# Kernel optimization log

Hardware: AMD Instinct MI355X
Metric: run time of the kernel (lower is better)

Reference implementation:

```python
import jax, jax.numpy as jnp
import numpy as np

CHANNELS = 64
WEIGHT_NUMS = [66 * 64, 64 * 64, 64]  # layer0 (C+2)->C, layer1 C->C, layer2 C->1
BIAS_NUMS = [64, 64, 1]
NUM_GEN_PARAMS = sum(WEIGHT_NUMS) + sum(BIAS_NUMS)  # 8513


def setup_inputs() -> dict:
    key = jax.random.key(0)
    k1, k2 = jax.random.split(key)
    N, C, H, W = 4, 64, 80, 200
    num_ins = 8  # instances per image -> M = 32 total
    M = N * num_ins
    x = jax.random.normal(k1, (N, C, H, W), dtype=jnp.float32)
    mask_head_params = jax.random.normal(k2, (M, NUM_GEN_PARAMS), dtype=jnp.float32) * 0.1
    return {"x": x, "mask_head_params": mask_head_params, "num_ins": num_ins}


def reference(x, mask_head_params, num_ins):
    N, C, H, W = x.shape
    ch = CHANNELS
    # compute_locations with stride=1 (stride//2 == 0); source bug divides the
    # whole tensor by W (locations[:1,:,:] /= W on a batch-1 tensor).
    xx, yy = jnp.meshgrid(jnp.arange(W, dtype=x.dtype), jnp.arange(H, dtype=x.dtype), indexing='xy')
    loc = jnp.stack([xx, yy], axis=0) / W  # [2, H, W]
    xa = jnp.concatenate([jnp.broadcast_to(loc[None], (N, 2, H, W)), x], axis=1)  # [N, C+2, H, W]
    feats = jnp.repeat(xa, num_ins, axis=0)  # [M, C+2, H, W] per-instance inputs
    M = feats.shape[0]
    # parse_dynamic_params: split generated params into per-layer weights/biases
    splits = np.cumsum(WEIGHT_NUMS + BIAS_NUMS)[:-1]
    w0, w1, w2, b0, b1, b2 = jnp.split(mask_head_params, splits, axis=1)
    w0 = w0.reshape(M, ch, ch + 2)
    w1 = w1.reshape(M, ch, ch)
    w2 = w2.reshape(M, 1, ch)
    b2 = b2 - 2.19  # mask bias shift (is_mask=True)
    # grouped 1x1 convs (groups=M) as per-instance GEMMs with ReLU between layers
    h = jax.nn.relu(jnp.einsum('mkc,mchw->mkhw', w0, feats) + b0[:, :, None, None])
    h = jax.nn.relu(jnp.einsum('mkc,mchw->mkhw', w1, h) + b1[:, :, None, None])
    out = jnp.einsum('mkc,mchw->mkhw', w2, h) + b2[:, :, None, None]
    return out.reshape(1, -1, H, W)  # [1, M*out_channels, H, W]
```

## Files before the change

kernel.cpp:

```cpp
#include <hip/hip_runtime.h>

typedef __attribute__((ext_vector_type(8))) short    short8;
typedef __attribute__((ext_vector_type(4))) float    f32x4;
typedef __attribute__((ext_vector_type(4))) unsigned uint4_;
typedef __attribute__((ext_vector_type(2))) unsigned uint2_;

#define HW     16000
#define WWID   200
#define NPARAM 8513

__device__ __forceinline__ unsigned f2bf(float f) {
    unsigned u = __builtin_bit_cast(unsigned, f);
    return (u + 0x7FFFu + ((u >> 16) & 1u)) >> 16;
}
__device__ __forceinline__ unsigned pkbf2(float a, float b) {
    return f2bf(a) | (f2bf(b) << 16);
}
__device__ __forceinline__ short8 mk8(unsigned a, unsigned b, unsigned c, unsigned d) {
    uint4_ u; u.x = a; u.y = b; u.z = c; u.w = d;
    return __builtin_bit_cast(short8, u);
}

__global__ __launch_bounds__(512, 1) void condlane_fused(
    const float* __restrict__ x,
    const float* __restrict__ params,
    float* __restrict__ out,
    int num_ins)
{
    extern __shared__ char lds[];
    char* xt = lds;
    const int tid  = threadIdx.x;
    const int lane = tid & 63;
    const int wid  = tid >> 6;
    const int n    = blockIdx.y;
    const int pxg0 = blockIdx.x * 256;
    char* h0a = lds + 65536 + wid * 4096;
    char* h0b = h0a + 2048;

    {
        const int p   = tid & 255;
        const int sel = tid >> 8;
        const int pc  = min(pxg0 + p, HW - 1);
        const float* xp = x + (size_t)n * 64 * HW + pc;
        #pragma unroll
        for (int it = 0; it < 4; ++it) {
            int c0 = sel * 32 + it * 8;
            uint4_ d;
            d.x = pkbf2(xp[(size_t)(c0 + 0) * HW], xp[(size_t)(c0 + 1) * HW]);
            d.y = pkbf2(xp[(size_t)(c0 + 2) * HW], xp[(size_t)(c0 + 3) * HW]);
            d.z = pkbf2(xp[(size_t)(c0 + 4) * HW], xp[(size_t)(c0 + 5) * HW]);
            d.w = pkbf2(xp[(size_t)(c0 + 6) * HW], xp[(size_t)(c0 + 7) * HW]);
            int byte = (p * 256 + c0 * 2) ^ ((p & 15) << 4);
            *(uint4_*)(xt + byte) = d;
        }
        const int pg = pxg0 + p;
        float lx = (float)(pg % WWID) * (1.0f / WWID);
        float ly = (float)(pg / WWID) * (1.0f / WWID);
        uint4_ z; z.x = 0; z.y = 0; z.z = 0; z.w = 0;
        uint4_ cv; cv.x = pkbf2(lx, ly); cv.y = pkbf2(1.0f, 0.0f); cv.z = 0; cv.w = 0;
        int ba = (p * 256 + 128 + sel * 32) ^ ((p & 15) << 4);
        int bb = (p * 256 + 144 + sel * 32) ^ ((p & 15) << 4);
        *(uint4_*)(xt + ba) = (sel == 0) ? cv : z;
        *(uint4_*)(xt + bb) = z;
    }

    const int m  = n * num_ins + wid;
    const int g  = (lane >> 4) & 3;
    const int hi = lane >> 4;
    const float* pm = params + (size_t)m * NPARAM;

    short8 w0f[3][4], w1f[2][4];
    #pragma unroll
    for (int kb = 0; kb < 4; ++kb) {
        const int k = kb * 16 + (lane & 15);
        #pragma unroll
        for (int ch = 0; ch < 2; ++ch) {
            const float* s = pm + k * 66 + 2 + ch * 32 + hi * 8;
            w0f[ch][kb] = mk8(pkbf2(s[0], s[1]), pkbf2(s[2], s[3]),
                              pkbf2(s[4], s[5]), pkbf2(s[6], s[7]));
        }
        {
            float a = (hi == 0) ? pm[k * 66 + 0] : 0.0f;
            float b = (hi == 0) ? pm[k * 66 + 1] : 0.0f;
            float c = (hi == 0) ? pm[8384 + k]   : 0.0f;
            w0f[2][kb] = mk8(pkbf2(a, b), pkbf2(c, 0.0f), 0u, 0u);
        }
        #pragma unroll
        for (int ch = 0; ch < 2; ++ch) {
            const float* s = pm + 4224 + k * 64 + ch * 32 + hi * 8;
            w1f[ch][kb] = mk8(pkbf2(s[0], s[1]), pkbf2(s[2], s[3]),
                              pkbf2(s[4], s[5]), pkbf2(s[6], s[7]));
        }
    }
    f32x4 bias1[4], w2v[4];
    #pragma unroll
    for (int kb = 0; kb < 4; ++kb)
        #pragma unroll
        for (int j = 0; j < 4; ++j) {
            bias1[kb][j] = pm[8448 + kb * 16 + g * 4 + j];
            w2v[kb][j]   = pm[8320 + kb * 16 + g * 4 + j];
        }
    const float b2 = pm[8512] - 2.19f;

    __syncthreads();

    const int nsl = min(16, (HW - pxg0) >> 4);
    const int hpx = lane & 15;
    const int swz = (lane & 15) << 4;

    for (int sA = 0; sA < 8; ++sA) {
        const int sB = sA + 8;
        const int pxlA = sA * 16 + hpx;
        const int pxlB = pxlA + 128;
        short8 xfA[3], xfB[3];
        #pragma unroll
        for (int ch = 0; ch < 3; ++ch) {
            xfA[ch] = *(const short8*)(xt + ((pxlA * 256 + ch * 64 + hi * 16) ^ swz));
            xfB[ch] = *(const short8*)(xt + ((pxlB * 256 + ch * 64 + hi * 16) ^ swz));
        }
        f32x4 acc0A[4], acc0B[4];
        #pragma unroll
        for (int kb = 0; kb < 4; ++kb)
            #pragma unroll
            for (int j = 0; j < 4; ++j) { acc0A[kb][j] = 0.f; acc0B[kb][j] = 0.f; }
        #pragma unroll
        for (int ch = 0; ch < 3; ++ch)
            #pragma unroll
            for (int kb = 0; kb < 4; ++kb) {
                acc0A[kb] = __builtin_amdgcn_mfma_f32_16x16x32_bf16(w0f[ch][kb], xfA[ch], acc0A[kb], 0, 0, 0);
                acc0B[kb] = __builtin_amdgcn_mfma_f32_16x16x32_bf16(w0f[ch][kb], xfB[ch], acc0B[kb], 0, 0, 0);
            }
        #pragma unroll
        for (int kb = 0; kb < 4; ++kb) {
            uint2_ pkA, pkB;
            pkA.x = pkbf2(fmaxf(acc0A[kb][0], 0.f), fmaxf(acc0A[kb][1], 0.f));
            pkA.y = pkbf2(fmaxf(acc0A[kb][2], 0.f), fmaxf(acc0A[kb][3], 0.f));
            pkB.x = pkbf2(fmaxf(acc0B[kb][0], 0.f), fmaxf(acc0B[kb][1], 0.f));
            pkB.y = pkbf2(fmaxf(acc0B[kb][2], 0.f), fmaxf(acc0B[kb][3], 0.f));
            int byte = (hpx * 128 + kb * 32 + g * 8) ^ ((hpx & 7) << 4);
            *(uint2_*)(h0a + byte) = pkA;
            *(uint2_*)(h0b + byte) = pkB;
        }
        short8 hfA[2], hfB[2];
        #pragma unroll
        for (int ch = 0; ch < 2; ++ch) {
            int byte = (hpx * 128 + ch * 64 + hi * 16) ^ ((hpx & 7) << 4);
            hfA[ch] = *(const short8*)(h0a + byte);
            hfB[ch] = *(const short8*)(h0b + byte);
        }
        f32x4 acc1A[4], acc1B[4];
        #pragma unroll
        for (int kb = 0; kb < 4; ++kb) { acc1A[kb] = bias1[kb]; acc1B[kb] = bias1[kb]; }
        #pragma unroll
        for (int ch = 0; ch < 2; ++ch)
            #pragma unroll
            for (int kb = 0; kb < 4; ++kb) {
                acc1A[kb] = __builtin_amdgcn_mfma_f32_16x16x32_bf16(w1f[ch][kb], hfA[ch], acc1A[kb], 0, 0, 0);
                acc1B[kb] = __builtin_amdgcn_mfma_f32_16x16x32_bf16(w1f[ch][kb], hfB[ch], acc1B[kb], 0, 0, 0);
            }
        float vA = 0.f, vB = 0.f;
        #pragma unroll
        for (int kb = 0; kb < 4; ++kb)
            #pragma unroll
            for (int j = 0; j < 4; ++j) {
                vA += w2v[kb][j] * fmaxf(acc1A[kb][j], 0.f);
                vB += w2v[kb][j] * fmaxf(acc1B[kb][j], 0.f);
            }
        vA += __shfl_xor(vA, 16); vA += __shfl_xor(vA, 32);
        vB += __shfl_xor(vB, 16); vB += __shfl_xor(vB, 32);
        if (lane < 16)
            out[(size_t)m * HW + pxg0 + sA * 16 + lane] = vA + b2;
        else if (lane < 32 && sB < nsl)
            out[(size_t)m * HW + pxg0 + sB * 16 + (lane - 16)] = vB + b2;
    }
}

extern "C" void kernel_launch(void* const* d_in, const int* in_sizes, int n_in,
                              void* d_out, int out_size, void* d_ws, size_t ws_size,
                              hipStream_t stream) {
    const float* x      = (const float*)d_in[0];
    const float* params = (const float*)d_in[1];
    float* out          = (float*)d_out;

    const int N = in_sizes[0] / (64 * HW);
    const int M = in_sizes[1] / NPARAM;
    const int num_ins = M / N;

    dim3 grid((HW + 255) / 256, N);
    condlane_fused<<<grid, 512, 98304, stream>>>(x, params, out, num_ins);
}
```

Before: 26.30 us.

## Split output channels across wave pairs with 1024-thread blocks

Doubles the block to 16 waves, so each instance is handled by two waves that each own half of the 64 hidden channels. Layer-0 activations are exchanged through a double-buffered shared h0 tile, and partial layer-2 sums are combined through LDS with a one-step-delayed store. The aim is more waves in flight and fewer registers per wave, for better latency hiding. The cost is a block-wide __syncthreads every pixel slice, and only one 16-pixel slice is processed per iteration instead of two.

```diff
diff --git a/kernel.cpp b/kernel.cpp
--- a/kernel.cpp
+++ b/kernel.cpp
@@ -21,21 +21,26 @@
     return __builtin_bit_cast(short8, u);
 }
 
-__global__ __launch_bounds__(512, 1) void condlane_fused(
+__global__ __launch_bounds__(1024, 4) void condlane_ksplit(
     const float* __restrict__ x,
     const float* __restrict__ params,
     float* __restrict__ out,
-    int num_ins)
+    int num_ins, int M_total)
 {
     extern __shared__ char lds[];
-    char* xt = lds;
+    char*  xt     = lds;
+    char*  h0base = lds + 65536;
+    float* vpart  = (float*)(lds + 65536 + 32768);
+
     const int tid  = threadIdx.x;
     const int lane = tid & 63;
     const int wid  = tid >> 6;
+    const int inst = wid >> 1;
+    const int kh   = wid & 1;
     const int n    = blockIdx.y;
     const int pxg0 = blockIdx.x * 256;
-    char* h0a = lds + 65536 + wid * 4096;
-    char* h0b = h0a + 2048;
+    const int g    = (lane >> 4) & 3;
+    const int px16 = lane & 15;
 
     {
         const int p   = tid & 255;
@@ -43,8 +48,8 @@
         const int pc  = min(pxg0 + p, HW - 1);
         const float* xp = x + (size_t)n * 64 * HW + pc;
         #pragma unroll
-        for (int it = 0; it < 4; ++it) {
-            int c0 = sel * 32 + it * 8;
+        for (int it = 0; it < 2; ++it) {
+            int c0 = sel * 16 + it * 8;
             uint4_ d;
             d.x = pkbf2(xp[(size_t)(c0 + 0) * HW], xp[(size_t)(c0 + 1) * HW]);
             d.y = pkbf2(xp[(size_t)(c0 + 2) * HW], xp[(size_t)(c0 + 3) * HW]);
@@ -56,122 +61,117 @@
         const int pg = pxg0 + p;
         float lx = (float)(pg % WWID) * (1.0f / WWID);
         float ly = (float)(pg / WWID) * (1.0f / WWID);
-        uint4_ z; z.x = 0; z.y = 0; z.z = 0; z.w = 0;
-        uint4_ cv; cv.x = pkbf2(lx, ly); cv.y = pkbf2(1.0f, 0.0f); cv.z = 0; cv.w = 0;
-        int ba = (p * 256 + 128 + sel * 32) ^ ((p & 15) << 4);
-        int bb = (p * 256 + 144 + sel * 32) ^ ((p & 15) << 4);
-        *(uint4_*)(xt + ba) = (sel == 0) ? cv : z;
-        *(uint4_*)(xt + bb) = z;
+        uint4_ cv;
+        cv.x = (sel == 0) ? pkbf2(lx, ly)   : 0u;
+        cv.y = (sel == 0) ? pkbf2(1.f, 0.f) : 0u;
+        cv.z = 0u; cv.w = 0u;
+        int byte = (p * 256 + 128 + sel * 16) ^ ((p & 15) << 4);
+        *(uint4_*)(xt + byte) = cv;
     }
 
-    const int m  = n * num_ins + wid;
-    const int g  = (lane >> 4) & 3;
-    const int hi = lane >> 4;
-    const float* pm = params + (size_t)m * NPARAM;
+    const int m  = n * num_ins + inst;
+    const float* pm = params + (size_t)min(m, M_total - 1) * NPARAM;
 
-    short8 w0f[3][4], w1f[2][4];
+    short8 w0f[3][2], w1f[2][2];
     #pragma unroll
-    for (int kb = 0; kb < 4; ++kb) {
-        const int k = kb * 16 + (lane & 15);
+    for (int kbl = 0; kbl < 2; ++kbl) {
+        const int k = kh * 32 + kbl * 16 + px16;
         #pragma unroll
         for (int ch = 0; ch < 2; ++ch) {
-            const float* s = pm + k * 66 + 2 + ch * 32 + hi * 8;
-            w0f[ch][kb] = mk8(pkbf2(s[0], s[1]), pkbf2(s[2], s[3]),
-                              pkbf2(s[4], s[5]), pkbf2(s[6], s[7]));
+            const float* s0 = pm + k * 66 + 2 + ch * 32 + g * 8;
+            w0f[ch][kbl] = mk8(pkbf2(s0[0], s0[1]), pkbf2(s0[2], s0[3]),
+                               pkbf2(s0[4], s0[5]), pkbf2(s0[6], s0[7]));
+            const float* s1 = pm + 4224 + k * 64 + ch * 32 + g * 8;
+            w1f[ch][kbl] = mk8(pkbf2(s1[0], s1[1]), pkbf2(s1[2], s1[3]),
+                               pkbf2(s1[4], s1[5]), pkbf2(s1[6], s1[7]));
         }
-        {
-            float a = (hi == 0) ? pm[k * 66 + 0] : 0.0f;
-            float b = (hi == 0) ? pm[k * 66 + 1] : 0.0f;
-            float c = (hi == 0) ? pm[8384 + k]   : 0.0f;
-            w0f[2][kb] = mk8(pkbf2(a, b), pkbf2(c, 0.0f), 0u, 0u);
-        }
-        #pragma unroll
-        for (int ch = 0; ch < 2; ++ch) {
-            const float* s = pm + 4224 + k * 64 + ch * 32 + hi * 8;
-            w1f[ch][kb] = mk8(pkbf2(s[0], s[1]), pkbf2(s[2], s[3]),
-                              pkbf2(s[4], s[5]), pkbf2(s[6], s[7]));
-        }
+        float a = (g == 0) ? pm[k * 66 + 0] : 0.0f;
+        float b = (g == 0) ? pm[k * 66 + 1] : 0.0f;
+        float c = (g == 0) ? pm[8384 + k]   : 0.0f;
+        w0f[2][kbl] = mk8(pkbf2(a, b), pkbf2(c, 0.0f), 0u, 0u);
     }
-    f32x4 bias1[4], w2v[4];
+    f32x4 bias1[2], w2v[2];
     #pragma unroll
-    for (int kb = 0; kb < 4; ++kb)
+    for (int kbl = 0; kbl < 2; ++kbl)
         #pragma unroll
         for (int j = 0; j < 4; ++j) {
-            bias1[kb][j] = pm[8448 + kb * 16 + g * 4 + j];
-            w2v[kb][j]   = pm[8320 + kb * 16 + g * 4 + j];
+            bias1[kbl][j] = pm[8448 + kh * 32 + kbl * 16 + g * 4 + j];
+            w2v[kbl][j]   = pm[8320 + kh * 32 + kbl * 16 + g * 4 + j];
         }
     const float b2 = pm[8512] - 2.19f;
 
     __syncthreads();
 
-    const int nsl = min(16, (HW - pxg0) >> 4);
-    const int hpx = lane & 15;
-    const int swz = (lane & 15) << 4;
+    const int  swzx = px16 << 4;
+    const int  swzh = (px16 & 7) << 4;
+    const bool do_store = (kh == 0) && (lane < 16) && (inst < num_ins);
 
-    for (int sA = 0; sA < 8; ++sA) {
-        const int sB = sA + 8;
-        const int pxlA = sA * 16 + hpx;
-        const int pxlB = pxlA + 128;
-        short8 xfA[3], xfB[3];
+    for (int s = 0; s < 16; ++s) {
+        const int pxl = s * 16 + px16;
+        short8 xf[3];
         #pragma unroll
-        for (int ch = 0; ch < 3; ++ch) {
-            xfA[ch] = *(const short8*)(xt + ((pxlA * 256 + ch * 64 + hi * 16) ^ swz));
-            xfB[ch] = *(const short8*)(xt + ((pxlB * 256 + ch * 64 + hi * 16) ^ swz));
-        }
-        f32x4 acc0A[4], acc0B[4];
+        for (int ch = 0; ch < 3; ++ch)
+            xf[ch] = *(const short8*)(xt + ((pxl * 256 + ch * 64 + g * 16) ^ swzx));
+        f32x4 acc0[2];
         #pragma unroll
-        for (int kb = 0; kb < 4; ++kb)
+        for (int kbl = 0; kbl < 2; ++kbl)
             #pragma unroll
-            for (int j = 0; j < 4; ++j) { acc0A[kb][j] = 0.f; acc0B[kb][j] = 0.f; }
+            for (int j = 0; j < 4; ++j) acc0[kbl][j] = 0.f;
         #pragma unroll
         for (int ch = 0; ch < 3; ++ch)
             #pragma unroll
-            for (int kb = 0; kb < 4; ++kb) {
-                acc0A[kb] = __builtin_amdgcn_mfma_f32_16x16x32_bf16(w0f[ch][kb], xfA[ch], acc0A[kb], 0, 0, 0);
-                acc0B[kb] = __builtin_amdgcn_mfma_f32_16x16x32_bf16(w0f[ch][kb], xfB[ch], acc0B[kb], 0, 0, 0);
-            }
+            for (int kbl = 0; kbl < 2; ++kbl)
+                acc0[kbl] = __builtin_amdgcn_mfma_f32_16x16x32_bf16(w0f[ch][kbl], xf[ch], acc0[kbl], 0, 0, 0);
+        char* hb = h0base + (s & 1) * 16384 + inst * 2048;
         #pragma unroll
-        for (int kb = 0; kb < 4; ++kb) {
-            uint2_ pkA, pkB;
-            pkA.x = pkbf2(fmaxf(acc0A[kb][0], 0.f), fmaxf(acc0A[kb][1], 0.f));
-            pkA.y = pkbf2(fmaxf(acc0A[kb][2], 0.f), fmaxf(acc0A[kb][3], 0.f));
-            pkB.x = pkbf2(fmaxf(acc0B[kb][0], 0.f), fmaxf(acc0B[kb][1], 0.f));
-            pkB.y = pkbf2(fmaxf(acc0B[kb][2], 0.f), fmaxf(acc0B[kb][3], 0.f));
-            int byte = (hpx * 128 + kb * 32 + g * 8) ^ ((hpx & 7) << 4);
-            *(uint2_*)(h0a + byte) = pkA;
-            *(uint2_*)(h0b + byte) = pkB;
+        for (int kbl = 0; kbl < 2; ++kbl) {
+            uint2_ pk;
+            pk.x = pkbf2(fmaxf(acc0[kbl][0], 0.f), fmaxf(acc0[kbl][1], 0.f));
+            pk.y = pkbf2(fmaxf(acc0[kbl][2], 0.f), fmaxf(acc0[kbl][3], 0.f));
+            int c0 = kh * 32 + kbl * 16 + g * 4;
+            int byte = (px16 * 128 + c0 * 2) ^ swzh;
+            *(uint2_*)(hb + byte) = pk;
         }
-        short8 hfA[2], hfB[2];
+
+        __syncthreads();
+
+        if (s > 0 && do_store) {
+            const float* vp = vpart + ((s - 1) & 1) * 256 + inst * 32;
+            float v = vp[lane] + vp[16 + lane];
+            int pxg = pxg0 + (s - 1) * 16 + lane;
+            if (pxg < HW) out[(size_t)m * HW + pxg] = v + b2;
+        }
+
+        short8 hf[2];
         #pragma unroll
-        for (int ch = 0; ch < 2; ++ch) {
-            int byte = (hpx * 128 + ch * 64 + hi * 16) ^ ((hpx & 7) << 4);
-            hfA[ch] = *(const short8*)(h0a + byte);
-            hfB[ch] = *(const short8*)(h0b + byte);
-        }
-        f32x4 acc1A[4], acc1B[4];
+        for (int ch = 0; ch < 2; ++ch)
+            hf[ch] = *(const short8*)(hb + ((px16 * 128 + ch * 64 + g * 16) ^ swzh));
+        f32x4 acc1[2];
         #pragma unroll
-        for (int kb = 0; kb < 4; ++kb) { acc1A[kb] = bias1[kb]; acc1B[kb] = bias1[kb]; }
+        for (int kbl = 0; kbl < 2; ++kbl) acc1[kbl] = bias1[kbl];
         #pragma unroll
         for (int ch = 0; ch < 2; ++ch)
             #pragma unroll
-            for (int kb = 0; kb < 4; ++kb) {
-                acc1A[kb] = __builtin_amdgcn_mfma_f32_16x16x32_bf16(w1f[ch][kb], hfA[ch], acc1A[kb], 0, 0, 0);
-                acc1B[kb] = __builtin_amdgcn_mfma_f32_16x16x32_bf16(w1f[ch][kb], hfB[ch], acc1B[kb], 0, 0, 0);
-            }
-        float vA = 0.f, vB = 0.f;
+            for (int kbl = 0; kbl < 2; ++kbl)
+                acc1[kbl] = __builtin_amdgcn_mfma_f32_16x16x32_bf16(w1f[ch][kbl], hf[ch], acc1[kbl], 0, 0, 0);
+        float v = 0.f;
         #pragma unroll
-        for (int kb = 0; kb < 4; ++kb)
+        for (int kbl = 0; kbl < 2; ++kbl)
             #pragma unroll
-            for (int j = 0; j < 4; ++j) {
-                vA += w2v[kb][j] * fmaxf(acc1A[kb][j], 0.f);
-                vB += w2v[kb][j] * fmaxf(acc1B[kb][j], 0.f);
-            }
-        vA += __shfl_xor(vA, 16); vA += __shfl_xor(vA, 32);
-        vB += __shfl_xor(vB, 16); vB += __shfl_xor(vB, 32);
+            for (int j = 0; j < 4; ++j)
+                v += w2v[kbl][j] * fmaxf(acc1[kbl][j], 0.f);
+        v += __shfl_xor(v, 16);
+        v += __shfl_xor(v, 32);
         if (lane < 16)
-            out[(size_t)m * HW + pxg0 + sA * 16 + lane] = vA + b2;
-        else if (lane < 32 && sB < nsl)
-            out[(size_t)m * HW + pxg0 + sB * 16 + (lane - 16)] = vB + b2;
+            vpart[(s & 1) * 256 + inst * 32 + kh * 16 + lane] = v;
+    }
+
+    __syncthreads();
+    if (do_store) {
+        const float* vp = vpart + (15 & 1) * 256 + inst * 32;
+        float v = vp[lane] + vp[16 + lane];
+        int pxg = pxg0 + 15 * 16 + lane;
+        if (pxg < HW) out[(size_t)m * HW + pxg] = v + b2;
     }
 }
 
@@ -187,5 +187,5 @@
     const int num_ins = M / N;
 
     dim3 grid((HW + 255) / 256, N);
-    condlane_fused<<<grid, 512, 98304, stream>>>(x, params, out, num_ins);
+    condlane_ksplit<<<grid, 1024, 100352, stream>>>(x, params, out, num_ins, M);
 }
```

Result: slower. 28.06 us (+6.7%).
